# Kernel optimization log

Hardware: AMD Instinct MI355X
Metric: run time of the kernel (lower is better)

## Reference

```python
import jax, jax.numpy as jnp
import numpy as np

N = 8192
D = 128
DEG = 32
E = N * DEG
A = 64


def setup_inputs() -> dict:
    key = jax.random.key(0)
    ks = jax.random.split(key, 10)
    node_features = jax.random.normal(ks[0], (N, D), dtype=jnp.float32)
    edge_features = jax.random.normal(ks[1], (N, N), dtype=jnp.float32)
    # deterministic edge list (distinct (src,dst) pairs, consistent with an adjacency nonzero())
    src_idx = jnp.repeat(jnp.arange(N, dtype=jnp.int32), DEG)
    offs = (jnp.arange(DEG, dtype=jnp.int32) + 1) * 37  # 37*32 < N -> all offsets distinct mod N
    dst_idx = (src_idx + jnp.tile(offs, N)) % N
    # message MLP: Linear(2D+1 -> D)
    W_msg = jax.random.normal(ks[2], (D, 2 * D + 1), dtype=jnp.float32) / np.sqrt(2 * D + 1)
    b_msg = jax.random.normal(ks[3], (D,), dtype=jnp.float32) * 0.01
    # GRUCell(D, D): gates ordered r, z, n
    w_ih = jax.random.normal(ks[4], (3 * D, D), dtype=jnp.float32) / np.sqrt(D)
    w_hh = jax.random.normal(ks[5], (3 * D, D), dtype=jnp.float32) / np.sqrt(D)
    b_ih = jax.random.normal(ks[6], (3 * D,), dtype=jnp.float32) * 0.01
    b_hh = jax.random.normal(ks[7], (3 * D,), dtype=jnp.float32) * 0.01
    # policy readout
    W_pol = jax.random.normal(ks[8], (A, D), dtype=jnp.float32) / np.sqrt(D)
    b_pol = jax.random.normal(ks[9], (A,), dtype=jnp.float32) * 0.01
    return {"node_features": node_features, "edge_features": edge_features,
            "src_idx": src_idx, "dst_idx": dst_idx,
            "W_msg": W_msg, "b_msg": b_msg,
            "w_ih": w_ih, "w_hh": w_hh, "b_ih": b_ih, "b_hh": b_hh,
            "W_pol": W_pol, "b_pol": b_pol}


def reference(node_features, edge_features, src_idx, dst_idx,
              W_msg, b_msg, w_ih, w_hh, b_ih, b_hh, W_pol, b_pol):
    # NOTE: the source loop never reassigns node_features, so every iteration
    # computes the same updated_node_features; we mirror it literally.
    for _ in range(3):
        src = node_features[src_idx]                              # [E, D]
        dst = node_features[dst_idx]                              # [E, D]
        ef = edge_features[src_idx, dst_idx][:, None]             # [E, 1]
        combined = jnp.concatenate([src, dst, ef], axis=1)        # [E, 2D+1]
        messages = jax.nn.relu(combined @ W_msg.T + b_msg)        # [E, D]
        agg = jnp.zeros_like(node_features).at[dst_idx].add(messages)  # [N, D]
        # GRUCell(agg, node_features), torch gate order r, z, n
        gi = agg @ w_ih.T + b_ih                                  # [N, 3D]
        gh = node_features @ w_hh.T + b_hh                        # [N, 3D]
        i_r, i_z, i_n = jnp.split(gi, 3, axis=1)
        h_r, h_z, h_n = jnp.split(gh, 3, axis=1)
        r = jax.nn.sigmoid(i_r + h_r)
        z = jax.nn.sigmoid(i_z + h_z)
        n = jnp.tanh(i_n + r * h_n)
        updated = (1.0 - z) * n + z * node_features               # [N, D]
    node_sum = updated.sum(axis=0)                                # [D]
    return node_sum @ W_pol.T + b_pol                             # [A]
```

## Files before the change

### kernel.cpp

```cpp
#include <hip/hip_runtime.h>

#define NN 8192
#define DD 128
#define DEG 32
#define EE (NN*DEG)
#define AA 64
#define AGP 132

using short8 = __attribute__((ext_vector_type(8))) short;
using f32x4  = __attribute__((ext_vector_type(4))) float;

__device__ __forceinline__ unsigned short f2bf(float x) {
    unsigned u = __builtin_bit_cast(unsigned, x);
    u += 0x7FFFu + ((u >> 16) & 1u);
    return (unsigned short)(u >> 16);
}

__device__ __forceinline__ short8 ld8bf_v(const float* p) {
    const float4 v0 = *(const float4*)p;
    const float4 v1 = *(const float4*)(p + 4);
    short8 r;
    r[0] = (short)f2bf(v0.x); r[1] = (short)f2bf(v0.y);
    r[2] = (short)f2bf(v0.z); r[3] = (short)f2bf(v0.w);
    r[4] = (short)f2bf(v1.x); r[5] = (short)f2bf(v1.y);
    r[6] = (short)f2bf(v1.z); r[7] = (short)f2bf(v1.w);
    return r;
}
__device__ __forceinline__ short8 ld8bf_s(const float* p) {
    short8 r;
#pragma unroll
    for (int i = 0; i < 8; ++i) r[i] = (short)f2bf(p[i]);
    return r;
}


__global__ __launch_bounds__(256) void k1_kernel(
    const float* __restrict__ nf, const float* __restrict__ efeat,
    const int* __restrict__ src_idx, const int* __restrict__ dst_idx,
    const float* __restrict__ W_msg, const float* __restrict__ b_msg,
    int* __restrict__ inv_src, float* __restrict__ eft,
    float* __restrict__ P, float* __restrict__ Q,
    float* __restrict__ node_sum, float* __restrict__ w3f,
    int* __restrict__ done_ctr)
{
    const int t = threadIdx.x, b = blockIdx.x;
    if (b < 128) {
        const int w = t >> 6, l = t & 63, p = l & 15, q = l >> 4;
        const int rbase = b * 64 + (w & 1) * 32;
        const int nh = (w >> 1) * 4;
        f32x4 accP[2][4], accQ[2][4];
        const f32x4 z4 = {0.f, 0.f, 0.f, 0.f};
#pragma unroll
        for (int m = 0; m < 2; ++m)
#pragma unroll
            for (int n = 0; n < 4; ++n) { accP[m][n] = z4; accQ[m][n] = z4; }

        const float* arow0 = &nf[(size_t)(rbase + p) * DD];
        const float* arow1 = &nf[(size_t)(rbase + 16 + p) * DD];
#pragma unroll
        for (int ks = 0; ks < 4; ++ks) {
            const int ko = ks * 32 + q * 8;
            const short8 a0 = ld8bf_v(arow0 + ko);
            const short8 a1 = ld8bf_v(arow1 + ko);
#pragma unroll
            for (int ni = 0; ni < 4; ++ni) {
                const int wr = (nh + ni) * 16 + p;
                const short8 b1 = ld8bf_s(&W_msg[(size_t)wr * 257 + ko]);
                const short8 b2 = ld8bf_s(&W_msg[(size_t)wr * 257 + 128 + ko]);
                accP[0][ni] = __builtin_amdgcn_mfma_f32_16x16x32_bf16(a0, b1, accP[0][ni], 0, 0, 0);
                accP[1][ni] = __builtin_amdgcn_mfma_f32_16x16x32_bf16(a1, b1, accP[1][ni], 0, 0, 0);
                accQ[0][ni] = __builtin_amdgcn_mfma_f32_16x16x32_bf16(a0, b2, accQ[0][ni], 0, 0, 0);
                accQ[1][ni] = __builtin_amdgcn_mfma_f32_16x16x32_bf16(a1, b2, accQ[1][ni], 0, 0, 0);
            }
        }
#pragma unroll
        for (int ni = 0; ni < 4; ++ni) {
            const int col = (nh + ni) * 16 + p;
            const float bv = b_msg[col];
#pragma unroll
            for (int m = 0; m < 2; ++m)
#pragma unroll
                for (int r = 0; r < 4; ++r) {
                    const size_t row = rbase + m * 16 + q * 4 + r;
                    P[row * DD + col] = accP[m][ni][r];
                    Q[row * DD + col] = accQ[m][ni][r] + bv;
                }
        }
    } else {
        const int idx = (b - 128) * 256 + t;
        const int d = dst_idx[idx], s = src_idx[idx];
        const int slot = d * DEG + (idx & 31);
        inv_src[slot] = s;
        eft[slot] = efeat[(size_t)s * NN + d];
        if (idx < DD) { node_sum[idx] = 0.f; w3f[idx] = W_msg[idx * 257 + 256]; }
        if (idx == 128) *done_ctr = 0;
    }
}

__global__ __launch_bounds__(512) void k2_kernel(
    const float* __restrict__ nf,
    const float* __restrict__ w_ih, const float* __restrict__ w_hh,
    const float* __restrict__ b_ih, const float* __restrict__ b_hh,
    const float* __restrict__ W_pol, const float* __restrict__ b_pol,
    const int* __restrict__ inv_src, const float* __restrict__ eft,
    const float* __restrict__ P, const float* __restrict__ Q,
    const float* __restrict__ w3f, float* __restrict__ node_sum,
    int* __restrict__ done_ctr, float* __restrict__ out)
{
    __shared__ int   s_src[1024];
    __shared__ float s_ef[1024];
    __shared__ __align__(16) float aggs[32 * AGP];
    __shared__ int   s_last;
    __shared__ float s_ns[DD];

    const int t = threadIdx.x, b = blockIdx.x;
    const int n0 = b * 32;

    for (int i = t; i < 1024; i += 512) {
        s_src[i] = inv_src[n0 * DEG + i];
        s_ef[i]  = eft[n0 * DEG + i];
    }
    __syncthreads();

    {
        const float4* P4 = (const float4*)P;
        const float4* Q4 = (const float4*)Q;
        const int c = t & 31;
        const float4 w3v = ((const float4*)w3f)[c];
#pragma unroll
        for (int pass = 0; pass < 2; ++pass) {
            const int dl = pass * 16 + (t >> 5);
            const int d = n0 + dl;
            const float4 qv = Q4[(size_t)d * 32 + c];
            float ax = 0.f, ay = 0.f, az = 0.f, aw = 0.f;
#pragma unroll 4
            for (int j = 0; j < DEG; ++j) {
                const int s = s_src[dl * DEG + j];
                const float ef = s_ef[dl * DEG + j];
                const float4 pv = P4[(size_t)s * 32 + c];
                ax += fmaxf(pv.x + fmaf(ef, w3v.x, qv.x), 0.f);
                ay += fmaxf(pv.y + fmaf(ef, w3v.y, qv.y), 0.f);
                az += fmaxf(pv.z + fmaf(ef, w3v.z, qv.z), 0.f);
                aw += fmaxf(pv.w + fmaf(ef, w3v.w, qv.w), 0.f);
            }
            const float4 r4 = { ax, ay, az, aw };
            *(float4*)&aggs[dl * AGP + c * 4] = r4;
        }
    }
    __syncthreads();

    {
        const int w = t >> 6, l = t & 63, p = l & 15, q = l >> 4;
        const int col = w * 16 + p;
        f32x4 aR[2], aZ[2], aIN[2], aHN[2];
        const f32x4 z4 = {0.f, 0.f, 0.f, 0.f};
        aR[0] = z4; aR[1] = z4; aZ[0] = z4; aZ[1] = z4;
        aIN[0] = z4; aIN[1] = z4; aHN[0] = z4; aHN[1] = z4;
#pragma unroll
        for (int ks = 0; ks < 4; ++ks) {
            const int ko = ks * 32 + q * 8;
            const short8 g0 = ld8bf_v(&aggs[p * AGP + ko]);
            const short8 g1 = ld8bf_v(&aggs[(16 + p) * AGP + ko]);
            const short8 h0 = ld8bf_v(&nf[(size_t)(n0 + p) * DD + ko]);
            const short8 h1 = ld8bf_v(&nf[(size_t)(n0 + 16 + p) * DD + ko]);
            const short8 wir = ld8bf_v(&w_ih[(size_t)col * DD + ko]);
            const short8 whr = ld8bf_v(&w_hh[(size_t)col * DD + ko]);
            const short8 wiz = ld8bf_v(&w_ih[(size_t)(128 + col) * DD + ko]);
            const short8 whz = ld8bf_v(&w_hh[(size_t)(128 + col) * DD + ko]);
            const short8 win = ld8bf_v(&w_ih[(size_t)(256 + col) * DD + ko]);
            const short8 whn = ld8bf_v(&w_hh[(size_t)(256 + col) * DD + ko]);
            aR[0]  = __builtin_amdgcn_mfma_f32_16x16x32_bf16(g0, wir, aR[0], 0, 0, 0);
            aR[0]  = __builtin_amdgcn_mfma_f32_16x16x32_bf16(h0, whr, aR[0], 0, 0, 0);
            aR[1]  = __builtin_amdgcn_mfma_f32_16x16x32_bf16(g1, wir, aR[1], 0, 0, 0);
            aR[1]  = __builtin_amdgcn_mfma_f32_16x16x32_bf16(h1, whr, aR[1], 0, 0, 0);
            aZ[0]  = __builtin_amdgcn_mfma_f32_16x16x32_bf16(g0, wiz, aZ[0], 0, 0, 0);
            aZ[0]  = __builtin_amdgcn_mfma_f32_16x16x32_bf16(h0, whz, aZ[0], 0, 0, 0);
            aZ[1]  = __builtin_amdgcn_mfma_f32_16x16x32_bf16(g1, wiz, aZ[1], 0, 0, 0);
            aZ[1]  = __builtin_amdgcn_mfma_f32_16x16x32_bf16(h1, whz, aZ[1], 0, 0, 0);
            aIN[0] = __builtin_amdgcn_mfma_f32_16x16x32_bf16(g0, win, aIN[0], 0, 0, 0);
            aIN[1] = __builtin_amdgcn_mfma_f32_16x16x32_bf16(g1, win, aIN[1], 0, 0, 0);
            aHN[0] = __builtin_amdgcn_mfma_f32_16x16x32_bf16(h0, whn, aHN[0], 0, 0, 0);
            aHN[1] = __builtin_amdgcn_mfma_f32_16x16x32_bf16(h1, whn, aHN[1], 0, 0, 0);
        }
        const float cbr  = b_ih[col] + b_hh[col];
        const float cbz  = b_ih[128 + col] + b_hh[128 + col];
        const float cbin = b_ih[256 + col];
        const float cbhn = b_hh[256 + col];
        float sumv = 0.f;
#pragma unroll
        for (int m = 0; m < 2; ++m)
#pragma unroll
            for (int rr = 0; rr < 4; ++rr) {
                const int row = n0 + m * 16 + q * 4 + rr;
                const float r = 1.f / (1.f + expf(-(aR[m][rr] + cbr)));
                const float z = 1.f / (1.f + expf(-(aZ[m][rr] + cbz)));
                const float n = tanhf(aIN[m][rr] + cbin + r * (aHN[m][rr] + cbhn));
                const float h = nf[(size_t)row * DD + col];
                sumv += (1.f - z) * n + z * h;
            }
        sumv += __shfl_xor(sumv, 16);
        sumv += __shfl_xor(sumv, 32);
        if (q == 0) atomicAdd(&node_sum[col], sumv);
    }

    __threadfence();
    __syncthreads();
    if (t == 0) s_last = (atomicAdd(done_ctr, 1) == (int)gridDim.x - 1) ? 1 : 0;
    __syncthreads();
    if (s_last) {
        if (t < DD) s_ns[t] = atomicAdd(&node_sum[t], 0.f);
        __syncthreads();
        if (t < AA) {
            float s = b_pol[t];
#pragma unroll 4
            for (int k = 0; k < DD; ++k) s = fmaf(s_ns[k], W_pol[t * DD + k], s);
            out[t] = s;
        }
    }
}

extern "C" void kernel_launch(void* const* d_in, const int* in_sizes, int n_in,
                              void* d_out, int out_size, void* d_ws, size_t ws_size,
                              hipStream_t stream)
{
    const float* nf    = (const float*)d_in[0];
    const float* efeat = (const float*)d_in[1];
    const int*   src   = (const int*)d_in[2];
    const int*   dst   = (const int*)d_in[3];
    const float* W_msg = (const float*)d_in[4];
    const float* b_msg = (const float*)d_in[5];
    const float* w_ih  = (const float*)d_in[6];
    const float* w_hh  = (const float*)d_in[7];
    const float* b_ih  = (const float*)d_in[8];
    const float* b_hh  = (const float*)d_in[9];
    const float* W_pol = (const float*)d_in[10];
    const float* b_pol = (const float*)d_in[11];
    float* out = (float*)d_out;

    char* ws = (char*)d_ws;
    int*   inv_src  = (int*)(ws + 0);
    float* eft      = (float*)(ws + 1048576);
    float* P        = (float*)(ws + 2097152);
    float* Q        = (float*)(ws + 6291456);
    float* node_sum = (float*)(ws + 10485760);
    float* w3f      = (float*)(ws + 10486272);
    int*   done_ctr = (int*)(ws + 10486784);

    k1_kernel<<<128 + EE / 256, 256, 0, stream>>>(nf, efeat, src, dst, W_msg, b_msg,
                                                  inv_src, eft, P, Q, node_sum, w3f,
                                                  done_ctr);
    k2_kernel<<<NN / 32, 512, 0, stream>>>(nf, w_ih, w_hh, b_ih, b_hh, W_pol, b_pol,
                                           inv_src, eft, P, Q, w3f, node_sum,
                                           done_ctr, out);
}
```

Baseline: 87.92 us.

## Store P/Q/agg in bf16, split gather and GRU into separate kernels

The P and Q projections, the aggregated messages and the GRU weights are now stored as bf16 instead of fp32, which halves the bytes moved by the edge gather. The fused aggregation+GRU kernel is split into a gather kernel (two nodes per block, one feature per thread) and a GRU kernel where six waves each compute one gate matmul and stage results in LDS. In k1 the W_msg tile is converted once into LDS rather than being loaded and converted per MFMA. The split adds a kernel launch and an extra round trip of the aggregate through global memory, and the extra bf16 rounding of P/Q adds some numerical error.

```diff
diff --git a/kernel.cpp b/kernel.cpp
--- a/kernel.cpp
+++ b/kernel.cpp
@@ -5,7 +5,7 @@
 #define DEG 32
 #define EE (NN*DEG)
 #define AA 64
-#define AGP 132
+#define KP 136
 
 using short8 = __attribute__((ext_vector_type(8))) short;
 using f32x4  = __attribute__((ext_vector_type(4))) float;
@@ -15,7 +15,10 @@
     u += 0x7FFFu + ((u >> 16) & 1u);
     return (unsigned short)(u >> 16);
 }
-
+__device__ __forceinline__ float bf2f(unsigned short h) {
+    unsigned u = ((unsigned)h) << 16;
+    return __builtin_bit_cast(float, u);
+}
 __device__ __forceinline__ short8 ld8bf_v(const float* p) {
     const float4 v0 = *(const float4*)p;
     const float4 v1 = *(const float4*)(p + 4);
@@ -26,25 +29,34 @@
     r[6] = (short)f2bf(v1.z); r[7] = (short)f2bf(v1.w);
     return r;
 }
-__device__ __forceinline__ short8 ld8bf_s(const float* p) {
-    short8 r;
-#pragma unroll
-    for (int i = 0; i < 8; ++i) r[i] = (short)f2bf(p[i]);
-    return r;
-}
 
 
 __global__ __launch_bounds__(256) void k1_kernel(
     const float* __restrict__ nf, const float* __restrict__ efeat,
     const int* __restrict__ src_idx, const int* __restrict__ dst_idx,
     const float* __restrict__ W_msg, const float* __restrict__ b_msg,
+    const float* __restrict__ w_ih, const float* __restrict__ w_hh,
     int* __restrict__ inv_src, float* __restrict__ eft,
-    float* __restrict__ P, float* __restrict__ Q,
+    unsigned short* __restrict__ Pbf, unsigned short* __restrict__ Qbf,
+    unsigned short* __restrict__ wibf, unsigned short* __restrict__ whbf,
     float* __restrict__ node_sum, float* __restrict__ w3f,
     int* __restrict__ done_ctr)
 {
+    __shared__ __align__(16) unsigned short Ws[2][128 * KP];
     const int t = threadIdx.x, b = blockIdx.x;
+
     if (b < 128) {
+        for (int u = t; u < 4096; u += 256) {
+            const int f = u >> 5;
+            const int k4 = (u & 31) * 4;
+            const float* wr = &W_msg[(size_t)f * 257 + k4];
+            unsigned short h1[4] = { f2bf(wr[0]), f2bf(wr[1]), f2bf(wr[2]), f2bf(wr[3]) };
+            unsigned short h2[4] = { f2bf(wr[128]), f2bf(wr[129]), f2bf(wr[130]), f2bf(wr[131]) };
+            *(uint2*)&Ws[0][f * KP + k4] = *(uint2*)h1;
+            *(uint2*)&Ws[1][f * KP + k4] = *(uint2*)h2;
+        }
+        __syncthreads();
+
         const int w = t >> 6, l = t & 63, p = l & 15, q = l >> 4;
         const int rbase = b * 64 + (w & 1) * 32;
         const int nh = (w >> 1) * 4;
@@ -64,9 +76,9 @@
             const short8 a1 = ld8bf_v(arow1 + ko);
 #pragma unroll
             for (int ni = 0; ni < 4; ++ni) {
-                const int wr = (nh + ni) * 16 + p;
-                const short8 b1 = ld8bf_s(&W_msg[(size_t)wr * 257 + ko]);
-                const short8 b2 = ld8bf_s(&W_msg[(size_t)wr * 257 + 128 + ko]);
+                const int fr = (nh + ni) * 16 + p;
+                const short8 b1 = *(const short8*)&Ws[0][fr * KP + ko];
+                const short8 b2 = *(const short8*)&Ws[1][fr * KP + ko];
                 accP[0][ni] = __builtin_amdgcn_mfma_f32_16x16x32_bf16(a0, b1, accP[0][ni], 0, 0, 0);
                 accP[1][ni] = __builtin_amdgcn_mfma_f32_16x16x32_bf16(a1, b1, accP[1][ni], 0, 0, 0);
                 accQ[0][ni] = __builtin_amdgcn_mfma_f32_16x16x32_bf16(a0, b2, accQ[0][ni], 0, 0, 0);
@@ -82,8 +94,8 @@
 #pragma unroll
                 for (int r = 0; r < 4; ++r) {
                     const size_t row = rbase + m * 16 + q * 4 + r;
-                    P[row * DD + col] = accP[m][ni][r];
-                    Q[row * DD + col] = accQ[m][ni][r] + bv;
+                    Pbf[row * DD + col] = f2bf(accP[m][ni][r]);
+                    Qbf[row * DD + col] = f2bf(accQ[m][ni][r] + bv);
                 }
         }
     } else {
@@ -92,116 +104,113 @@
         const int slot = d * DEG + (idx & 31);
         inv_src[slot] = s;
         eft[slot] = efeat[(size_t)s * NN + d];
+        if (idx < 384 * DD) {
+            wibf[idx] = f2bf(w_ih[idx]);
+            whbf[idx] = f2bf(w_hh[idx]);
+        }
         if (idx < DD) { node_sum[idx] = 0.f; w3f[idx] = W_msg[idx * 257 + 256]; }
-        if (idx == 128) *done_ctr = 0;
-    }
-}
-
-__global__ __launch_bounds__(512) void k2_kernel(
-    const float* __restrict__ nf,
-    const float* __restrict__ w_ih, const float* __restrict__ w_hh,
+        if (idx == 200) *done_ctr = 0;
+    }
+}
+
+__global__ __launch_bounds__(256) void k2_kernel(
+    const unsigned short* __restrict__ Pbf, const unsigned short* __restrict__ Qbf,
+    const int* __restrict__ inv_src, const float* __restrict__ eft,
+    const float* __restrict__ w3f, unsigned short* __restrict__ aggbf)
+{
+    __shared__ int   s_src[2][DEG];
+    __shared__ float s_ef[2][DEG];
+    const int t = threadIdx.x, blk = blockIdx.x;
+
+    if (t < 64) {
+        const int dl = t >> 5, j = t & 31;
+        const int d = blk * 2 + dl;
+        s_src[dl][j] = inv_src[d * DEG + j];
+        s_ef[dl][j]  = eft[d * DEG + j];
+    }
+    __syncthreads();
+
+    const int dl = t >> 7;
+    const int f = t & 127;
+    const int d = blk * 2 + dl;
+    const float base = bf2f(Qbf[(size_t)d * DD + f]);
+    const float w3v = w3f[f];
+
+    float acc = 0.f;
+#pragma unroll
+    for (int j = 0; j < DEG; ++j) {
+        const int s = s_src[dl][j];
+        const float pv = bf2f(Pbf[(size_t)s * DD + f]);
+        acc += fmaxf(pv + fmaf(s_ef[dl][j], w3v, base), 0.f);
+    }
+    aggbf[(size_t)d * DD + f] = f2bf(acc);
+}
+
+__global__ __launch_bounds__(384) void k3_kernel(
+    const float* __restrict__ nf, const unsigned short* __restrict__ aggbf,
+    const unsigned short* __restrict__ wibf, const unsigned short* __restrict__ whbf,
     const float* __restrict__ b_ih, const float* __restrict__ b_hh,
     const float* __restrict__ W_pol, const float* __restrict__ b_pol,
-    const int* __restrict__ inv_src, const float* __restrict__ eft,
-    const float* __restrict__ P, const float* __restrict__ Q,
-    const float* __restrict__ w3f, float* __restrict__ node_sum,
-    int* __restrict__ done_ctr, float* __restrict__ out)
-{
-    __shared__ int   s_src[1024];
-    __shared__ float s_ef[1024];
-    __shared__ __align__(16) float aggs[32 * AGP];
+    float* __restrict__ node_sum, int* __restrict__ done_ctr,
+    float* __restrict__ out)
+{
+    __shared__ float gate_s[6][32][132];
     __shared__ int   s_last;
     __shared__ float s_ns[DD];
 
-    const int t = threadIdx.x, b = blockIdx.x;
-    const int n0 = b * 32;
-
-    for (int i = t; i < 1024; i += 512) {
-        s_src[i] = inv_src[n0 * DEG + i];
-        s_ef[i]  = eft[n0 * DEG + i];
-    }
-    __syncthreads();
-
-    {
-        const float4* P4 = (const float4*)P;
-        const float4* Q4 = (const float4*)Q;
-        const int c = t & 31;
-        const float4 w3v = ((const float4*)w3f)[c];
-#pragma unroll
-        for (int pass = 0; pass < 2; ++pass) {
-            const int dl = pass * 16 + (t >> 5);
-            const int d = n0 + dl;
-            const float4 qv = Q4[(size_t)d * 32 + c];
-            float ax = 0.f, ay = 0.f, az = 0.f, aw = 0.f;
-#pragma unroll 4
-            for (int j = 0; j < DEG; ++j) {
-                const int s = s_src[dl * DEG + j];
-                const float ef = s_ef[dl * DEG + j];
-                const float4 pv = P4[(size_t)s * 32 + c];
-                ax += fmaxf(pv.x + fmaf(ef, w3v.x, qv.x), 0.f);
-                ay += fmaxf(pv.y + fmaf(ef, w3v.y, qv.y), 0.f);
-                az += fmaxf(pv.z + fmaf(ef, w3v.z, qv.z), 0.f);
-                aw += fmaxf(pv.w + fmaf(ef, w3v.w, qv.w), 0.f);
-            }
-            const float4 r4 = { ax, ay, az, aw };
-            *(float4*)&aggs[dl * AGP + c * 4] = r4;
-        }
-    }
-    __syncthreads();
-
-    {
-        const int w = t >> 6, l = t & 63, p = l & 15, q = l >> 4;
-        const int col = w * 16 + p;
-        f32x4 aR[2], aZ[2], aIN[2], aHN[2];
-        const f32x4 z4 = {0.f, 0.f, 0.f, 0.f};
-        aR[0] = z4; aR[1] = z4; aZ[0] = z4; aZ[1] = z4;
-        aIN[0] = z4; aIN[1] = z4; aHN[0] = z4; aHN[1] = z4;
-#pragma unroll
-        for (int ks = 0; ks < 4; ++ks) {
-            const int ko = ks * 32 + q * 8;
-            const short8 g0 = ld8bf_v(&aggs[p * AGP + ko]);
-            const short8 g1 = ld8bf_v(&aggs[(16 + p) * AGP + ko]);
-            const short8 h0 = ld8bf_v(&nf[(size_t)(n0 + p) * DD + ko]);
-            const short8 h1 = ld8bf_v(&nf[(size_t)(n0 + 16 + p) * DD + ko]);
-            const short8 wir = ld8bf_v(&w_ih[(size_t)col * DD + ko]);
-            const short8 whr = ld8bf_v(&w_hh[(size_t)col * DD + ko]);
-            const short8 wiz = ld8bf_v(&w_ih[(size_t)(128 + col) * DD + ko]);
-            const short8 whz = ld8bf_v(&w_hh[(size_t)(128 + col) * DD + ko]);
-            const short8 win = ld8bf_v(&w_ih[(size_t)(256 + col) * DD + ko]);
-            const short8 whn = ld8bf_v(&w_hh[(size_t)(256 + col) * DD + ko]);
-            aR[0]  = __builtin_amdgcn_mfma_f32_16x16x32_bf16(g0, wir, aR[0], 0, 0, 0);
-            aR[0]  = __builtin_amdgcn_mfma_f32_16x16x32_bf16(h0, whr, aR[0], 0, 0, 0);
-            aR[1]  = __builtin_amdgcn_mfma_f32_16x16x32_bf16(g1, wir, aR[1], 0, 0, 0);
-            aR[1]  = __builtin_amdgcn_mfma_f32_16x16x32_bf16(h1, whr, aR[1], 0, 0, 0);
-            aZ[0]  = __builtin_amdgcn_mfma_f32_16x16x32_bf16(g0, wiz, aZ[0], 0, 0, 0);
-            aZ[0]  = __builtin_amdgcn_mfma_f32_16x16x32_bf16(h0, whz, aZ[0], 0, 0, 0);
-            aZ[1]  = __builtin_amdgcn_mfma_f32_16x16x32_bf16(g1, wiz, aZ[1], 0, 0, 0);
-            aZ[1]  = __builtin_amdgcn_mfma_f32_16x16x32_bf16(h1, whz, aZ[1], 0, 0, 0);
-            aIN[0] = __builtin_amdgcn_mfma_f32_16x16x32_bf16(g0, win, aIN[0], 0, 0, 0);
-            aIN[1] = __builtin_amdgcn_mfma_f32_16x16x32_bf16(g1, win, aIN[1], 0, 0, 0);
-            aHN[0] = __builtin_amdgcn_mfma_f32_16x16x32_bf16(h0, whn, aHN[0], 0, 0, 0);
-            aHN[1] = __builtin_amdgcn_mfma_f32_16x16x32_bf16(h1, whn, aHN[1], 0, 0, 0);
-        }
-        const float cbr  = b_ih[col] + b_hh[col];
-        const float cbz  = b_ih[128 + col] + b_hh[128 + col];
-        const float cbin = b_ih[256 + col];
-        const float cbhn = b_hh[256 + col];
-        float sumv = 0.f;
+    const int t = threadIdx.x;
+    const int n0 = blockIdx.x * 32;
+    const int wv = t >> 6, l = t & 63, p = l & 15, q = l >> 4;
+    const unsigned short* Wb = (wv < 3) ? wibf : whbf;
+    const int rowbase = (wv % 3) * 128;
+
+    f32x4 acc[2][8];
+    const f32x4 z4 = {0.f, 0.f, 0.f, 0.f};
+#pragma unroll
+    for (int n = 0; n < 8; ++n) { acc[0][n] = z4; acc[1][n] = z4; }
+
+#pragma unroll
+    for (int ks = 0; ks < 4; ++ks) {
+        const int ko = ks * 32 + q * 8;
+        short8 a0, a1;
+        if (wv < 3) {
+            a0 = *(const short8*)&aggbf[(size_t)(n0 + p) * DD + ko];
+            a1 = *(const short8*)&aggbf[(size_t)(n0 + 16 + p) * DD + ko];
+        } else {
+            a0 = ld8bf_v(&nf[(size_t)(n0 + p) * DD + ko]);
+            a1 = ld8bf_v(&nf[(size_t)(n0 + 16 + p) * DD + ko]);
+        }
+#pragma unroll
+        for (int n = 0; n < 8; ++n) {
+            const short8 bb = *(const short8*)&Wb[(size_t)(rowbase + n * 16 + p) * DD + ko];
+            acc[0][n] = __builtin_amdgcn_mfma_f32_16x16x32_bf16(a0, bb, acc[0][n], 0, 0, 0);
+            acc[1][n] = __builtin_amdgcn_mfma_f32_16x16x32_bf16(a1, bb, acc[1][n], 0, 0, 0);
+        }
+    }
+#pragma unroll
+    for (int n = 0; n < 8; ++n)
 #pragma unroll
         for (int m = 0; m < 2; ++m)
 #pragma unroll
-            for (int rr = 0; rr < 4; ++rr) {
-                const int row = n0 + m * 16 + q * 4 + rr;
-                const float r = 1.f / (1.f + expf(-(aR[m][rr] + cbr)));
-                const float z = 1.f / (1.f + expf(-(aZ[m][rr] + cbz)));
-                const float n = tanhf(aIN[m][rr] + cbin + r * (aHN[m][rr] + cbhn));
-                const float h = nf[(size_t)row * DD + col];
-                sumv += (1.f - z) * n + z * h;
-            }
-        sumv += __shfl_xor(sumv, 16);
-        sumv += __shfl_xor(sumv, 32);
-        if (q == 0) atomicAdd(&node_sum[col], sumv);
-    }
+            for (int r = 0; r < 4; ++r)
+                gate_s[wv][m * 16 + q * 4 + r][n * 16 + p] = acc[m][n][r];
+    __syncthreads();
+
+    const int f = t & 127;
+    const int g3 = t >> 7;
+    const float bir = b_ih[f], biz = b_ih[128 + f], bin = b_ih[256 + f];
+    const float bhr = b_hh[f], bhz = b_hh[128 + f], bhn = b_hh[256 + f];
+    float uloc = 0.f;
+    for (int j = g3; j < 32; j += 3) {
+        const float ir = gate_s[0][j][f], iz = gate_s[1][j][f], inn = gate_s[2][j][f];
+        const float hr = gate_s[3][j][f], hz = gate_s[4][j][f], hn = gate_s[5][j][f];
+        const float h = nf[(size_t)(n0 + j) * DD + f];
+        const float r = 1.f / (1.f + expf(-(ir + bir + hr + bhr)));
+        const float z = 1.f / (1.f + expf(-(iz + biz + hz + bhz)));
+        const float n = tanhf(inn + bin + r * (hn + bhn));
+        uloc += (1.f - z) * n + z * h;
+    }
+    atomicAdd(&node_sum[f], uloc);
 
     __threadfence();
     __syncthreads();
@@ -238,18 +247,21 @@
     float* out = (float*)d_out;
 
     char* ws = (char*)d_ws;
-    int*   inv_src  = (int*)(ws + 0);
-    float* eft      = (float*)(ws + 1048576);
-    float* P        = (float*)(ws + 2097152);
-    float* Q        = (float*)(ws + 6291456);
-    float* node_sum = (float*)(ws + 10485760);
-    float* w3f      = (float*)(ws + 10486272);
-    int*   done_ctr = (int*)(ws + 10486784);
+    int*            inv_src  = (int*)(ws + 0);
+    float*          eft      = (float*)(ws + 1048576);
+    unsigned short* Pbf      = (unsigned short*)(ws + 2097152);
+    unsigned short* Qbf      = (unsigned short*)(ws + 4194304);
+    unsigned short* aggbf    = (unsigned short*)(ws + 6291456);
+    unsigned short* wibf     = (unsigned short*)(ws + 8388608);
+    unsigned short* whbf     = (unsigned short*)(ws + 8486912);
+    float*          node_sum = (float*)(ws + 8585216);
+    float*          w3f      = (float*)(ws + 8585728);
+    int*            done_ctr = (int*)(ws + 8586240);
 
     k1_kernel<<<128 + EE / 256, 256, 0, stream>>>(nf, efeat, src, dst, W_msg, b_msg,
-                                                  inv_src, eft, P, Q, node_sum, w3f,
-                                                  done_ctr);
-    k2_kernel<<<NN / 32, 512, 0, stream>>>(nf, w_ih, w_hh, b_ih, b_hh, W_pol, b_pol,
-                                           inv_src, eft, P, Q, w3f, node_sum,
-                                           done_ctr, out);
-}
+                                                  w_ih, w_hh, inv_src, eft, Pbf, Qbf,
+                                                  wibf, whbf, node_sum, w3f, done_ctr);
+    k2_kernel<<<NN / 2, 256, 0, stream>>>(Pbf, Qbf, inv_src, eft, w3f, aggbf);
+    k3_kernel<<<NN / 32, 384, 0, stream>>>(nf, aggbf, wibf, whbf, b_ih, b_hh,
+                                           W_pol, b_pol, node_sum, done_ctr, out);
+}
```

Result: faster. 73.64 us (-16.2%).
